# Kernel optimization log

Measured on AMD Instinct MI355X. Metric: run time of the kernel, lower is better.

Reference implementation:

```python
import jax, jax.numpy as jnp
import numpy as np

B, S, M, D, H, L, FF = 2, 1024, 1024, 512, 8, 4, 2048
HD = D // H  # head dim 64
EPS = 1e-6   # fast_transformers linear-attention eps
LN_EPS = 1e-5


def setup_inputs() -> dict:
    key = jax.random.key(0)
    keys = iter(jax.random.split(key, 64))
    def w(shape, s=0.02):
        return jax.random.normal(next(keys), shape, dtype=jnp.float32) * s
    inp = {
        "memory": jax.random.normal(next(keys), (B, M, D), dtype=jnp.float32),
        "target": jax.random.normal(next(keys), (B, S, D), dtype=jnp.float32),
    }
    for p in ("sa", "ca"):
        for n in ("q", "k", "v", "o"):
            inp[f"{p}_W{n}"] = w((L, D, D))
            inp[f"{p}_b{n}"] = jnp.zeros((L, D), jnp.float32)
    inp["ff_W1"] = w((L, D, FF)); inp["ff_b1"] = jnp.zeros((L, FF), jnp.float32)
    inp["ff_W2"] = w((L, FF, D)); inp["ff_b2"] = jnp.zeros((L, D), jnp.float32)
    for n in ("ln1", "ln2", "ln3"):
        inp[f"{n}_g"] = jnp.ones((L, D), jnp.float32)
        inp[f"{n}_b"] = jnp.zeros((L, D), jnp.float32)
    inp["lnf_g"] = jnp.ones((D,), jnp.float32)
    inp["lnf_b"] = jnp.zeros((D,), jnp.float32)
    return inp


def _ln(x, g, b):
    m = x.mean(-1, keepdims=True)
    v = ((x - m) ** 2).mean(-1, keepdims=True)
    return (x - m) / jnp.sqrt(v + LN_EPS) * g + b


def _phi(x):  # elu feature map: elu(x) + 1
    return jax.nn.elu(x) + 1.0


def _heads(x, W, b):  # [b,s,D] -> [b,s,H,HD]
    y = x @ W + b
    return y.reshape(y.shape[0], y.shape[1], H, HD)


def _causal_linear_attn(q, k, v):
    # q,k already feature-mapped. cumulative KV state per step.
    kv = jnp.cumsum(jnp.einsum('bshd,bshm->bshdm', k, v), axis=1)  # [B,S,H,HD,HD]
    z = jnp.cumsum(k, axis=1)                                      # [B,S,H,HD]
    num = jnp.einsum('bshd,bshdm->bshm', q, kv)
    den = jnp.einsum('bshd,bshd->bsh', q, z) + EPS
    return num / den[..., None]


def _cross_linear_attn(q, k, v):
    kv = jnp.einsum('bmhd,bmhv->bhdv', k, v)  # [B,H,HD,HD]
    z = k.sum(axis=1)                          # [B,H,HD]
    num = jnp.einsum('bshd,bhdv->bshv', q, kv)
    den = jnp.einsum('bshd,bhd->bsh', q, z) + EPS
    return num / den[..., None]


def reference(memory, target,
              sa_Wq, sa_bq, sa_Wk, sa_bk, sa_Wv, sa_bv, sa_Wo, sa_bo,
              ca_Wq, ca_bq, ca_Wk, ca_bk, ca_Wv, ca_bv, ca_Wo, ca_bo,
              ff_W1, ff_b1, ff_W2, ff_b2,
              ln1_g, ln1_b, ln2_g, ln2_b, ln3_g, ln3_b, lnf_g, lnf_b):
    x = target
    for i in range(L):
        # causal linear self-attention
        q = _phi(_heads(x, sa_Wq[i], sa_bq[i]))
        k = _phi(_heads(x, sa_Wk[i], sa_bk[i]))
        v = _heads(x, sa_Wv[i], sa_bv[i])
        a = _causal_linear_attn(q, k, v).reshape(B, S, D) @ sa_Wo[i] + sa_bo[i]
        x = _ln(x + a, ln1_g[i], ln1_b[i])
        # linear cross-attention over memory
        q = _phi(_heads(x, ca_Wq[i], ca_bq[i]))
        k = _phi(_heads(memory, ca_Wk[i], ca_bk[i]))
        v = _heads(memory, ca_Wv[i], ca_bv[i])
        a = _cross_linear_attn(q, k, v).reshape(B, S, D) @ ca_Wo[i] + ca_bo[i]
        x = _ln(x + a, ln2_g[i], ln2_b[i])
        # gelu FFN
        y = jax.nn.gelu(x @ ff_W1[i] + ff_b1[i], approximate=False) @ ff_W2[i] + ff_b2[i]
        x = _ln(x + y, ln3_g[i], ln3_b[i])
    return _ln(x, lnf_g, lnf_b)
```

## Files before the change

### kernel.cpp

```cpp
#include <hip/hip_runtime.h>
#include <hip/hip_bf16.h>
#include <math.h>


typedef unsigned short u16;
typedef __bf16 bf16x8 __attribute__((ext_vector_type(8)));
typedef float f32x4v __attribute__((ext_vector_type(4)));
typedef long long i64;

#define DEVI __device__ __forceinline__

DEVI float bf2f(u16 u) { return __uint_as_float(((unsigned)u) << 16); }
DEVI u16 f2bf(float f) {
  unsigned u = __float_as_uint(f);
  u += 0x7FFFu + ((u >> 16) & 1u);
  return (u16)(u >> 16);
}

struct P8i { const float* p[8]; };
struct P8o { u16* p[8]; };

__global__ __launch_bounds__(256) void transpose_b8(P8i in, P8o out)
{
  __shared__ float tile[64 * 65];
  const int m = blockIdx.z;
  const int set = m >> 2, layer = m & 3;
  const float* src = in.p[set] + (size_t)layer * 512 * 512;
  u16* dst = out.p[set] + (size_t)layer * 512 * 512;
  const int n0 = blockIdx.x * 64, k0 = blockIdx.y * 64;
  const int t = threadIdx.x;
#pragma unroll
  for (int p = 0; p < 16; ++p) {
    const int e = t + p * 256;
    const int lk = e >> 6, ln = e & 63;
    tile[lk * 65 + ln] = src[(size_t)(k0 + lk) * 512 + n0 + ln];
  }
  __syncthreads();
#pragma unroll
  for (int p = 0; p < 16; ++p) {
    const int e = t + p * 256;
    const int ln = e >> 6, lk = e & 63;
    dst[(size_t)(n0 + ln) * 512 + k0 + lk] = f2bf(tile[lk * 65 + ln]);
  }
}

__global__ __launch_bounds__(256) void transpose_f2b(
    const float* __restrict__ in, u16* __restrict__ out, int K, int N)
{
  __shared__ float tile[64 * 65];
  const size_t mat = (size_t)blockIdx.z * K * N;
  const int n0 = blockIdx.x * 64, k0 = blockIdx.y * 64;
  const int t = threadIdx.x;
#pragma unroll
  for (int p = 0; p < 16; ++p) {
    const int e = t + p * 256;
    const int lk = e >> 6, ln = e & 63;
    tile[lk * 65 + ln] = in[mat + (size_t)(k0 + lk) * N + n0 + ln];
  }
  __syncthreads();
#pragma unroll
  for (int p = 0; p < 16; ++p) {
    const int e = t + p * 256;
    const int ln = e >> 6, lk = e & 63;
    out[mat + (size_t)(n0 + ln) * K + k0 + lk] = f2bf(tile[lk * 65 + ln]);
  }
}

__global__ __launch_bounds__(256) void cast_dual(
    const float* __restrict__ in, float* __restrict__ fout, u16* __restrict__ bout)
{
  const int i = blockIdx.x * 256 + threadIdx.x;
  const float4 a = ((const float4*)in)[i * 2];
  const float4 b = ((const float4*)in)[i * 2 + 1];
  if (fout) {
    ((float4*)fout)[i * 2] = a;
    ((float4*)fout)[i * 2 + 1] = b;
  }
  ((ushort4*)bout)[i * 2]     = make_ushort4(f2bf(a.x), f2bf(a.y), f2bf(a.z), f2bf(a.w));
  ((ushort4*)bout)[i * 2 + 1] = make_ushort4(f2bf(b.x), f2bf(b.y), f2bf(b.z), f2bf(b.w));
}

template<int CDT>
__global__ __launch_bounds__(256, 4) void gemm64(
    const u16* __restrict__ A0, const u16* __restrict__ A1, const u16* __restrict__ A2,
    const u16* __restrict__ W0, const u16* __restrict__ W1, const u16* __restrict__ W2,
    const float* __restrict__ b0, const float* __restrict__ b1, const float* __restrict__ b2,
    void* __restrict__ C0, void* __restrict__ C1, void* __restrict__ C2,
    int acts, int N, int K, int lda, int ldw, int lognyb,
    i64 zA, i64 zW, i64 zB, i64 zC, int biasAllZ)
{
  constexpr int LDT = 72;
  __shared__ __align__(16) u16 As[2][64 * LDT];
  __shared__ __align__(16) u16 Bs[2][64 * LDT];
  const int tid = threadIdx.x;
  const int by = blockIdx.y;
  const int z = blockIdx.z;
  const int seg = by >> lognyb;
  const int ny = by & ((1 << lognyb) - 1);
  const u16* A = (seg == 0 ? A0 : (seg == 1 ? A1 : A2)) + (size_t)z * zA;
  const u16* W = (seg == 0 ? W0 : (seg == 1 ? W1 : W2)) + (size_t)z * zW;
  const float* bias = (seg == 0 ? b0 : (seg == 1 ? b1 : b2)) + (size_t)z * zB;
  void* Cv = seg == 0 ? C0 : (seg == 1 ? C1 : C2);
  const int act = (acts >> (2 * seg)) & 3;
  const bool dobias = biasAllZ || (z == 0);

  const int bm0 = blockIdx.x * 64, bn0 = ny * 64;
  const int lane = tid & 63, wid = tid >> 6;
  const int wr = wid >> 1, wc = wid & 1;
  const int l15 = lane & 15, lg = lane >> 4;
  const int srow = tid >> 2, scg = (tid & 3) * 16;
  const u16* Ap = A + (size_t)(bm0 + srow) * lda + scg;
  const u16* Wp = W + (size_t)(bn0 + srow) * ldw + scg;
  const int nk = K >> 6;

  uint4 a00, a01, b00, b01;
  uint4 a10, a11, b10, b11;
#define LDSET0(k) { a00 = *(const uint4*)(Ap + (k) * 64); a01 = *(const uint4*)(Ap + (k) * 64 + 8); \
                    b00 = *(const uint4*)(Wp + (k) * 64); b01 = *(const uint4*)(Wp + (k) * 64 + 8); }
#define LDSET1(k) { a10 = *(const uint4*)(Ap + (k) * 64); a11 = *(const uint4*)(Ap + (k) * 64 + 8); \
                    b10 = *(const uint4*)(Wp + (k) * 64); b11 = *(const uint4*)(Wp + (k) * 64 + 8); }
#define STSET0(buf) { *(uint4*)&As[buf][srow * LDT + scg] = a00; *(uint4*)&As[buf][srow * LDT + scg + 8] = a01; \
                      *(uint4*)&Bs[buf][srow * LDT + scg] = b00; *(uint4*)&Bs[buf][srow * LDT + scg + 8] = b01; }
#define STSET1(buf) { *(uint4*)&As[buf][srow * LDT + scg] = a10; *(uint4*)&As[buf][srow * LDT + scg + 8] = a11; \
                      *(uint4*)&Bs[buf][srow * LDT + scg] = b10; *(uint4*)&Bs[buf][srow * LDT + scg + 8] = b11; }

  f32x4v acc[2][2] = {};
  auto mfma_on = [&](int buf) {
    bf16x8 af[2][2], bw[2][2];
#pragma unroll
    for (int kk = 0; kk < 2; ++kk) {
#pragma unroll
      for (int mm = 0; mm < 2; ++mm)
        af[kk][mm] = *(const bf16x8*)&As[buf][(wr * 32 + mm * 16 + l15) * LDT + kk * 32 + lg * 8];
#pragma unroll
      for (int nn = 0; nn < 2; ++nn)
        bw[kk][nn] = *(const bf16x8*)&Bs[buf][(wc * 32 + nn * 16 + l15) * LDT + kk * 32 + lg * 8];
    }
#pragma unroll
    for (int kk = 0; kk < 2; ++kk)
#pragma unroll
      for (int mm = 0; mm < 2; ++mm)
#pragma unroll
        for (int nn = 0; nn < 2; ++nn)
          acc[mm][nn] = __builtin_amdgcn_mfma_f32_16x16x32_bf16(af[kk][mm], bw[kk][nn], acc[mm][nn], 0, 0, 0);
  };

  LDSET0(0); STSET0(0);
  LDSET1(1);
  __syncthreads();
  for (int k = 0; k < nk; k += 2) {
    if (k + 2 < nk) LDSET0(k + 2);
    mfma_on(0);
    STSET1(1);
    __syncthreads();
    if (k + 3 < nk) LDSET1(k + 3);
    mfma_on(1);
    if (k + 2 < nk) STSET0(0);
    __syncthreads();
  }
#undef LDSET0
#undef LDSET1
#undef STSET0
#undef STSET1
#pragma unroll
  for (int nn = 0; nn < 2; ++nn) {
    const int col = bn0 + wc * 32 + nn * 16 + l15;
    const float bv = dobias ? bias[col] : 0.f;
#pragma unroll
    for (int mm = 0; mm < 2; ++mm) {
#pragma unroll
      for (int r = 0; r < 4; ++r) {
        const int row = bm0 + wr * 32 + mm * 16 + lg * 4 + r;
        float v = acc[mm][nn][r] + bv;
        if (act == 1) v = v > 0.f ? v + 1.f : __expf(v);
        else if (act == 2) v = 0.5f * v * (1.f + erff(v * 0.70710678f));
        const size_t idx = (size_t)row * N + col + (size_t)z * zC;
        if (CDT == 0) ((float*)Cv)[idx] = v;
        else          ((u16*)Cv)[idx] = f2bf(v);
      }
    }
  }
}

__global__ __launch_bounds__(256) void lin_chunk_mfma(
    const u16* __restrict__ kbuf, const u16* __restrict__ vbuf,
    float* __restrict__ KVc, float* __restrict__ zc)
{
  constexpr int LDT = 72;
  __shared__ __align__(16) u16 Kt[64 * LDT];
  __shared__ __align__(16) u16 Vt[64 * LDT];
  const int c = blockIdx.x, bh = blockIdx.y, zl = blockIdx.z;
  kbuf += (size_t)zl * 2048 * 512;
  vbuf += (size_t)zl * 2048 * 512;
  KVc  += (size_t)zl * 16 * 16 * 4096;
  zc   += (size_t)zl * 16 * 16 * 64;
  const int b = bh >> 3, h = bh & 7;
  const int t = threadIdx.x;
  const size_t rowbase = (size_t)(b * 1024 + c * 64);
  const int sp = t >> 4, colq = (t & 15) * 4;
#pragma unroll
  for (int pp = 0; pp < 2; ++pp) {
    const int s0 = pp * 32 + 2 * sp;
    const ushort4 ka = *(const ushort4*)&kbuf[(rowbase + s0) * 512 + h * 64 + colq];
    const ushort4 kb_ = *(const ushort4*)&kbuf[(rowbase + s0 + 1) * 512 + h * 64 + colq];
    const ushort4 va = *(const ushort4*)&vbuf[(rowbase + s0) * 512 + h * 64 + colq];
    const ushort4 vb_ = *(const ushort4*)&vbuf[(rowbase + s0 + 1) * 512 + h * 64 + colq];
    *(unsigned*)&Kt[(colq + 0) * LDT + s0] = (unsigned)ka.x | ((unsigned)kb_.x << 16);
    *(unsigned*)&Kt[(colq + 1) * LDT + s0] = (unsigned)ka.y | ((unsigned)kb_.y << 16);
    *(unsigned*)&Kt[(colq + 2) * LDT + s0] = (unsigned)ka.z | ((unsigned)kb_.z << 16);
    *(unsigned*)&Kt[(colq + 3) * LDT + s0] = (unsigned)ka.w | ((unsigned)kb_.w << 16);
    *(unsigned*)&Vt[(colq + 0) * LDT + s0] = (unsigned)va.x | ((unsigned)vb_.x << 16);
    *(unsigned*)&Vt[(colq + 1) * LDT + s0] = (unsigned)va.y | ((unsigned)vb_.y << 16);
    *(unsigned*)&Vt[(colq + 2) * LDT + s0] = (unsigned)va.z | ((unsigned)vb_.z << 16);
    *(unsigned*)&Vt[(colq + 3) * LDT + s0] = (unsigned)va.w | ((unsigned)vb_.w << 16);
  }
  __syncthreads();
  {
    const int zd = t >> 2, zg = t & 3;
    float zp = 0.f;
#pragma unroll
    for (int ss = 0; ss < 16; ++ss) zp += bf2f(Kt[zd * LDT + zg * 16 + ss]);
    zp += __shfl_xor(zp, 1, 64);
    zp += __shfl_xor(zp, 2, 64);
    if (zg == 0) zc[(size_t)(bh * 16 + c) * 64 + zd] = zp;
  }
  const int lane = t & 63, wid = t >> 6;
  const int wr = wid >> 1, wc = wid & 1;
  const int l15 = lane & 15, lg = lane >> 4;
  bf16x8 av[2][2], bk[2][2];
#pragma unroll
  for (int kk = 0; kk < 2; ++kk) {
#pragma unroll
    for (int mm = 0; mm < 2; ++mm)
      av[kk][mm] = *(const bf16x8*)&Vt[(wr * 32 + mm * 16 + l15) * LDT + kk * 32 + lg * 8];
#pragma unroll
    for (int nn = 0; nn < 2; ++nn)
      bk[kk][nn] = *(const bf16x8*)&Kt[(wc * 32 + nn * 16 + l15) * LDT + kk * 32 + lg * 8];
  }
  f32x4v acc[2][2] = {};
#pragma unroll
  for (int kk = 0; kk < 2; ++kk)
#pragma unroll
    for (int mm = 0; mm < 2; ++mm)
#pragma unroll
      for (int nn = 0; nn < 2; ++nn)
        acc[mm][nn] = __builtin_amdgcn_mfma_f32_16x16x32_bf16(av[kk][mm], bk[kk][nn], acc[mm][nn], 0, 0, 0);
  float* kvout = KVc + (size_t)(bh * 16 + c) * 4096;
#pragma unroll
  for (int mm = 0; mm < 2; ++mm)
#pragma unroll
    for (int r = 0; r < 4; ++r) {
      const int row = wr * 32 + mm * 16 + lg * 4 + r;
#pragma unroll
      for (int nn = 0; nn < 2; ++nn) {
        const int col = wc * 32 + nn * 16 + l15;
        kvout[row * 64 + col] = acc[mm][nn][r];
      }
    }
}

__global__ __launch_bounds__(256) void sa_apply_mfma(
    const u16* __restrict__ qbuf, const u16* __restrict__ kbuf,
    const u16* __restrict__ vbuf, const float* __restrict__ KVc,
    const float* __restrict__ zc, u16* __restrict__ out)
{
  constexpr int LDT = 72;
  __shared__ __align__(16) u16 Qs[64 * LDT];
  __shared__ __align__(16) u16 Ks[64 * LDT];
  __shared__ __align__(16) u16 Vt[64 * LDT];
  __shared__ __align__(16) u16 Ps[64 * LDT];
  __shared__ __align__(16) u16 KVs[64 * LDT];
  __shared__ float zp[64];
  __shared__ float den1[2][64];
  __shared__ float den2[64];
  const int c = blockIdx.x, bh = blockIdx.y;
  const int b = bh >> 3, h = bh & 7;
  const int t = threadIdx.x;
  const size_t rowbase = (size_t)(b * 1024 + c * 64);
  {
    const int srow = t >> 2, scg = (t & 3) * 16;
    *(uint4*)&Qs[srow * LDT + scg]     = *(const uint4*)&qbuf[(rowbase + srow) * 512 + h * 64 + scg];
    *(uint4*)&Qs[srow * LDT + scg + 8] = *(const uint4*)&qbuf[(rowbase + srow) * 512 + h * 64 + scg + 8];
    *(uint4*)&Ks[srow * LDT + scg]     = *(const uint4*)&kbuf[(rowbase + srow) * 512 + h * 64 + scg];
    *(uint4*)&Ks[srow * LDT + scg + 8] = *(const uint4*)&kbuf[(rowbase + srow) * 512 + h * 64 + scg + 8];
    const float* kvbase = KVc + (size_t)(bh * 16) * 4096 + srow * 64 + scg;
    float4 s0 = make_float4(0, 0, 0, 0), s1 = s0, s2 = s0, s3 = s0;
    for (int cc = 0; cc < c; ++cc) {
      const float* p = kvbase + (size_t)cc * 4096;
      const float4 a0 = *(const float4*)&p[0];
      const float4 a1 = *(const float4*)&p[4];
      const float4 a2 = *(const float4*)&p[8];
      const float4 a3 = *(const float4*)&p[12];
      s0.x += a0.x; s0.y += a0.y; s0.z += a0.z; s0.w += a0.w;
      s1.x += a1.x; s1.y += a1.y; s1.z += a1.z; s1.w += a1.w;
      s2.x += a2.x; s2.y += a2.y; s2.z += a2.z; s2.w += a2.w;
      s3.x += a3.x; s3.y += a3.y; s3.z += a3.z; s3.w += a3.w;
    }
    *(ushort4*)&KVs[srow * LDT + scg + 0]  = make_ushort4(f2bf(s0.x), f2bf(s0.y), f2bf(s0.z), f2bf(s0.w));
    *(ushort4*)&KVs[srow * LDT + scg + 4]  = make_ushort4(f2bf(s1.x), f2bf(s1.y), f2bf(s1.z), f2bf(s1.w));
    *(ushort4*)&KVs[srow * LDT + scg + 8]  = make_ushort4(f2bf(s2.x), f2bf(s2.y), f2bf(s2.z), f2bf(s2.w));
    *(ushort4*)&KVs[srow * LDT + scg + 12] = make_ushort4(f2bf(s3.x), f2bf(s3.y), f2bf(s3.z), f2bf(s3.w));
  }
  {
    const int sp = t >> 4, colq = (t & 15) * 4;
#pragma unroll
    for (int pp = 0; pp < 2; ++pp) {
      const int s0 = pp * 32 + 2 * sp;
      const ushort4 va = *(const ushort4*)&vbuf[(rowbase + s0) * 512 + h * 64 + colq];
      const ushort4 vb_ = *(const ushort4*)&vbuf[(rowbase + s0 + 1) * 512 + h * 64 + colq];
      *(unsigned*)&Vt[(colq + 0) * LDT + s0] = (unsigned)va.x | ((unsigned)vb_.x << 16);
      *(unsigned*)&Vt[(colq + 1) * LDT + s0] = (unsigned)va.y | ((unsigned)vb_.y << 16);
// ... 52 lines not shown
        dsum += val;
      }
      dsum += __shfl_xor(dsum, 1, 64);
      dsum += __shfl_xor(dsum, 2, 64);
      dsum += __shfl_xor(dsum, 4, 64);
      dsum += __shfl_xor(dsum, 8, 64);
      if (l15 == 0) den1[wc][row] = dsum;
    }
  __syncthreads();
  bf16x8 ap[2][2];
#pragma unroll
  for (int kk = 0; kk < 2; ++kk) {
#pragma unroll
    for (int mm = 0; mm < 2; ++mm)
      ap[kk][mm] = *(const bf16x8*)&Ps[(wr * 32 + mm * 16 + l15) * LDT + kk * 32 + lg * 8];
#pragma unroll
    for (int nn = 0; nn < 2; ++nn)
      bx[kk][nn] = *(const bf16x8*)&Vt[(wc * 32 + nn * 16 + l15) * LDT + kk * 32 + lg * 8];
  }
  f32x4v o_acc[2][2] = {};
#pragma unroll
  for (int kk = 0; kk < 2; ++kk)
#pragma unroll
    for (int mm = 0; mm < 2; ++mm)
#pragma unroll
      for (int nn = 0; nn < 2; ++nn)
        o_acc[mm][nn] = __builtin_amdgcn_mfma_f32_16x16x32_bf16(ap[kk][mm], bx[kk][nn], o_acc[mm][nn], 0, 0, 0);
#pragma unroll
  for (int kk = 0; kk < 2; ++kk)
#pragma unroll
    for (int nn = 0; nn < 2; ++nn)
      bx[kk][nn] = *(const bf16x8*)&KVs[(wc * 32 + nn * 16 + l15) * LDT + kk * 32 + lg * 8];
#pragma unroll
  for (int kk = 0; kk < 2; ++kk)
#pragma unroll
    for (int mm = 0; mm < 2; ++mm)
#pragma unroll
      for (int nn = 0; nn < 2; ++nn)
        o_acc[mm][nn] = __builtin_amdgcn_mfma_f32_16x16x32_bf16(af_q[kk][mm], bx[kk][nn], o_acc[mm][nn], 0, 0, 0);
#pragma unroll
  for (int mm = 0; mm < 2; ++mm)
#pragma unroll
    for (int r = 0; r < 4; ++r) {
      const int row = wr * 32 + mm * 16 + lg * 4 + r;
      const float rden = 1.f / (den1[0][row] + den1[1][row] + den2[row] + 1e-6f);
#pragma unroll
      for (int nn = 0; nn < 2; ++nn) {
        const int col = wc * 32 + nn * 16 + l15;
        out[(rowbase + row) * 512 + h * 64 + col] = f2bf(o_acc[mm][nn][r] * rden);
      }
    }
}

__global__ __launch_bounds__(256) void ca_apply_mfma(
    const float* __restrict__ qp0, i64 qstride, const float* __restrict__ KVc,
    const float* __restrict__ zc, u16* __restrict__ out)
{
  constexpr int LDT = 72;
  __shared__ __align__(16) u16 Qs[64 * LDT];
  __shared__ __align__(16) u16 KVs[64 * LDT];
  __shared__ float zt[64];
  __shared__ float den2[64];
  const int c = blockIdx.x, bh = blockIdx.y;
  const int b = bh >> 3, h = bh & 7;
  const int t = threadIdx.x;
  const size_t rowbase = (size_t)(b * 1024 + c * 64);
  {
    const int srow = t >> 2, scg = (t & 3) * 16;
    const float* qa = qp0 + (rowbase + srow) * 512 + h * 64 + scg;
    const float* qb = qa + qstride;
#pragma unroll
    for (int i = 0; i < 4; ++i) {
      const float4 u = *(const float4*)&qa[i * 4];
      const float4 w = *(const float4*)&qb[i * 4];
      float e0 = u.x + w.x, e1 = u.y + w.y, e2 = u.z + w.z, e3 = u.w + w.w;
      e0 = e0 > 0.f ? e0 + 1.f : __expf(e0);
      e1 = e1 > 0.f ? e1 + 1.f : __expf(e1);
      e2 = e2 > 0.f ? e2 + 1.f : __expf(e2);
      e3 = e3 > 0.f ? e3 + 1.f : __expf(e3);
      *(ushort4*)&Qs[srow * LDT + scg + i * 4] = make_ushort4(f2bf(e0), f2bf(e1), f2bf(e2), f2bf(e3));
    }
    const float* kvbase = KVc + (size_t)(bh * 16) * 4096 + srow * 64 + scg;
    float4 s0 = make_float4(0, 0, 0, 0), s1 = s0, s2 = s0, s3 = s0;
    for (int cc = 0; cc < 16; ++cc) {
      const float* p = kvbase + (size_t)cc * 4096;
      const float4 a0 = *(const float4*)&p[0];
      const float4 a1 = *(const float4*)&p[4];
      const float4 a2 = *(const float4*)&p[8];
      const float4 a3 = *(const float4*)&p[12];
      s0.x += a0.x; s0.y += a0.y; s0.z += a0.z; s0.w += a0.w;
      s1.x += a1.x; s1.y += a1.y; s1.z += a1.z; s1.w += a1.w;
      s2.x += a2.x; s2.y += a2.y; s2.z += a2.z; s2.w += a2.w;
      s3.x += a3.x; s3.y += a3.y; s3.z += a3.z; s3.w += a3.w;
    }
    *(ushort4*)&KVs[srow * LDT + scg + 0]  = make_ushort4(f2bf(s0.x), f2bf(s0.y), f2bf(s0.z), f2bf(s0.w));
    *(ushort4*)&KVs[srow * LDT + scg + 4]  = make_ushort4(f2bf(s1.x), f2bf(s1.y), f2bf(s1.z), f2bf(s1.w));
    *(ushort4*)&KVs[srow * LDT + scg + 8]  = make_ushort4(f2bf(s2.x), f2bf(s2.y), f2bf(s2.z), f2bf(s2.w));
    *(ushort4*)&KVs[srow * LDT + scg + 12] = make_ushort4(f2bf(s3.x), f2bf(s3.y), f2bf(s3.z), f2bf(s3.w));
  }
  if (t < 64) {
    float z = 0.f;
    for (int cc = 0; cc < 16; ++cc) z += zc[(size_t)(bh * 16 + cc) * 64 + t];
    zt[t] = z;
  }
  __syncthreads();
  {
    const int di = t >> 2, dg = t & 3;
    float p2 = 0.f;
#pragma unroll
    for (int dd = 0; dd < 16; ++dd)
      p2 += bf2f(Qs[di * LDT + dg * 16 + dd]) * zt[dg * 16 + dd];
    p2 += __shfl_xor(p2, 1, 64);
    p2 += __shfl_xor(p2, 2, 64);
    if (dg == 0) den2[di] = p2;
  }
  const int lane = t & 63, wid = t >> 6;
  const int wr = wid >> 1, wc = wid & 1;
  const int l15 = lane & 15, lg = lane >> 4;
  bf16x8 aq[2][2], bkv[2][2];
#pragma unroll
  for (int kk = 0; kk < 2; ++kk) {
#pragma unroll
    for (int mm = 0; mm < 2; ++mm)
      aq[kk][mm] = *(const bf16x8*)&Qs[(wr * 32 + mm * 16 + l15) * LDT + kk * 32 + lg * 8];
#pragma unroll
    for (int nn = 0; nn < 2; ++nn)
      bkv[kk][nn] = *(const bf16x8*)&KVs[(wc * 32 + nn * 16 + l15) * LDT + kk * 32 + lg * 8];
  }
  f32x4v o_acc[2][2] = {};
#pragma unroll
  for (int kk = 0; kk < 2; ++kk)
#pragma unroll
    for (int mm = 0; mm < 2; ++mm)
#pragma unroll
      for (int nn = 0; nn < 2; ++nn)
        o_acc[mm][nn] = __builtin_amdgcn_mfma_f32_16x16x32_bf16(aq[kk][mm], bkv[kk][nn], o_acc[mm][nn], 0, 0, 0);
  __syncthreads();
#pragma unroll
  for (int mm = 0; mm < 2; ++mm)
#pragma unroll
    for (int r = 0; r < 4; ++r) {
      const int row = wr * 32 + mm * 16 + lg * 4 + r;
      const float rden = 1.f / (den2[row] + 1e-6f);
#pragma unroll
      for (int nn = 0; nn < 2; ++nn) {
        const int col = wc * 32 + nn * 16 + l15;
        out[(rowbase + row) * 512 + h * 64 + col] = f2bf(o_acc[mm][nn][r] * rden);
      }
    }
}

template<int NPART>
__global__ __launch_bounds__(256) void ln_residual(
    float* __restrict__ x, const float* __restrict__ a, i64 pstride,
    const float* __restrict__ g, const float* __restrict__ bt,
    u16* __restrict__ xb)
{
  const int t = threadIdx.x, lane = t & 63, w = t >> 6;
  const int row = blockIdx.x * 4 + w;
  float* xr = x + (size_t)row * 512;
  float4 x0 = *(const float4*)&xr[lane * 8];
  float4 x1 = *(const float4*)&xr[lane * 8 + 4];
  float v[8] = { x0.x, x0.y, x0.z, x0.w, x1.x, x1.y, x1.z, x1.w };
#pragma unroll
  for (int p = 0; p < NPART; ++p) {
    const float* ar = a + (size_t)p * pstride + (size_t)row * 512;
    float4 a0 = *(const float4*)&ar[lane * 8];
    float4 a1 = *(const float4*)&ar[lane * 8 + 4];
    v[0] += a0.x; v[1] += a0.y; v[2] += a0.z; v[3] += a0.w;
    v[4] += a1.x; v[5] += a1.y; v[6] += a1.z; v[7] += a1.w;
  }
  float s = 0.f, sq = 0.f;
#pragma unroll
  for (int i = 0; i < 8; ++i) { s += v[i]; sq += v[i] * v[i]; }
#pragma unroll
  for (int off = 32; off > 0; off >>= 1) {
    s += __shfl_xor(s, off, 64);
    sq += __shfl_xor(sq, off, 64);
  }
  const float mean = s * (1.f / 512.f);
  const float var = sq * (1.f / 512.f) - mean * mean;
  const float rstd = rsqrtf(var + 1e-5f);
  float o[8];
#pragma unroll
  for (int i = 0; i < 8; ++i) {
    const int col = lane * 8 + i;
    o[i] = (v[i] - mean) * rstd * g[col] + bt[col];
  }
  *(float4*)&xr[lane * 8]     = make_float4(o[0], o[1], o[2], o[3]);
  *(float4*)&xr[lane * 8 + 4] = make_float4(o[4], o[5], o[6], o[7]);
  *(ushort4*)&xb[(size_t)row * 512 + lane * 8]     = make_ushort4(f2bf(o[0]), f2bf(o[1]), f2bf(o[2]), f2bf(o[3]));
  *(ushort4*)&xb[(size_t)row * 512 + lane * 8 + 4] = make_ushort4(f2bf(o[4]), f2bf(o[5]), f2bf(o[6]), f2bf(o[7]));
}

__global__ __launch_bounds__(256) void ln_final(
    const float* __restrict__ x, const float* __restrict__ g,
    const float* __restrict__ bt, float* __restrict__ out)
{
  const int t = threadIdx.x, lane = t & 63, w = t >> 6;
  const int row = blockIdx.x * 4 + w;
  const float* xr = x + (size_t)row * 512;
  float4 x0 = *(const float4*)&xr[lane * 8];
  float4 x1 = *(const float4*)&xr[lane * 8 + 4];
  float v[8] = { x0.x, x0.y, x0.z, x0.w, x1.x, x1.y, x1.z, x1.w };
// ... 11 lines not shown
  float o[8];
#pragma unroll
  for (int i = 0; i < 8; ++i) {
    const int col = lane * 8 + i;
    o[i] = (v[i] - mean) * rstd * g[col] + bt[col];
  }
  *(float4*)&out[(size_t)row * 512 + lane * 8]     = make_float4(o[0], o[1], o[2], o[3]);
  *(float4*)&out[(size_t)row * 512 + lane * 8 + 4] = make_float4(o[4], o[5], o[6], o[7]);
}

extern "C" void kernel_launch(void* const* d_in, const int* in_sizes, int n_in,
                              void* d_out, int out_size, void* d_ws, size_t ws_size,
                              hipStream_t stream)
{
  (void)in_sizes; (void)n_in; (void)out_size; (void)ws_size;
  constexpr int Dm = 512, Lc = 4, FFc = 2048;
  constexpr i64 TOK = 2048LL * 512;

  const float* memory = (const float*)d_in[0];
  const float* target = (const float*)d_in[1];
  const float *saW[4], *sab[4], *caW[4], *cab[4];
  for (int j = 0; j < 4; ++j) {
    saW[j] = (const float*)d_in[2 + 2 * j];
    sab[j] = (const float*)d_in[3 + 2 * j];
    caW[j] = (const float*)d_in[10 + 2 * j];
    cab[j] = (const float*)d_in[11 + 2 * j];
  }
  const float* ffW1 = (const float*)d_in[18];
  const float* ffb1 = (const float*)d_in[19];
  const float* ffW2 = (const float*)d_in[20];
  const float* ffb2 = (const float*)d_in[21];
  const float* lng[4] = { (const float*)d_in[22], (const float*)d_in[24],
                          (const float*)d_in[26], (const float*)d_in[28] };
  const float* lnb[4] = { (const float*)d_in[23], (const float*)d_in[25],
                          (const float*)d_in[27], (const float*)d_in[29] };

  size_t off = 0;
  auto alloc = [&](size_t bytes) -> void* {
    void* p = (char*)d_ws + off;
    off += (bytes + 255) & ~(size_t)255;
    return p;
  };
  u16* WtS[4]; u16* WtC[4];
  for (int j = 0; j < 4; ++j) WtS[j] = (u16*)alloc((size_t)Lc * Dm * Dm * 2);
  for (int j = 0; j < 4; ++j) WtC[j] = (u16*)alloc((size_t)Lc * Dm * Dm * 2);
  u16* WtF1 = (u16*)alloc((size_t)Lc * Dm * FFc * 2);
  u16* WtF2 = (u16*)alloc((size_t)Lc * FFc * Dm * 2);
  float* x     = (float*)alloc(TOK * 4);
  u16*   xb    = (u16*)alloc(TOK * 2);
  u16*   memb  = (u16*)alloc(TOK * 2);
  u16*   qh    = (u16*)alloc(TOK * 2);
  u16*   kh    = (u16*)alloc(TOK * 2);
  u16*   vh    = (u16*)alloc(TOK * 2);
  u16*   khAll = (u16*)alloc((size_t)Lc * TOK * 2);
  u16*   vhAll = (u16*)alloc((size_t)Lc * TOK * 2);
  float* resid = (float*)alloc((size_t)4 * TOK * 4);
  u16*   attn  = (u16*)alloc(TOK * 2);
  u16*   ffh   = (u16*)alloc((size_t)2048 * 2048 * 2);
  float* KVc   = (float*)alloc((size_t)16 * 16 * 4096 * 4);
  float* zcb   = (float*)alloc((size_t)16 * 16 * 64 * 4);
  float* KVcA  = (float*)alloc((size_t)Lc * 16 * 16 * 4096 * 4);
  float* zcbA  = (float*)alloc((size_t)Lc * 16 * 16 * 64 * 4);

  {
    P8i pin; P8o pout;
    for (int j = 0; j < 4; ++j) { pin.p[j] = saW[j]; pout.p[j] = WtS[j]; }
    for (int j = 0; j < 4; ++j) { pin.p[4 + j] = caW[j]; pout.p[4 + j] = WtC[j]; }
    transpose_b8<<<dim3(8, 8, 32), 256, 0, stream>>>(pin, pout);
  }
  transpose_f2b<<<dim3(32, 8, 4), 256, 0, stream>>>(ffW1, WtF1, Dm, FFc);
  transpose_f2b<<<dim3(8, 32, 4), 256, 0, stream>>>(ffW2, WtF2, FFc, Dm);

  cast_dual<<<512, 256, 0, stream>>>(target, x, xb);
  cast_dual<<<512, 256, 0, stream>>>(memory, nullptr, memb);

  gemm64<1><<<dim3(32, 16, 4), 256, 0, stream>>>(
      memb, memb, memb, WtC[1], WtC[2], WtC[2],
      cab[1], cab[2], cab[2], khAll, vhAll, vhAll,
      0x01, 512, 512, 512, 512, 3,
      0, (i64)Dm * Dm, (i64)Dm, TOK, 1);
  lin_chunk_mfma<<<dim3(16, 16, 4), 256, 0, stream>>>(khAll, vhAll, KVcA, zcbA);

  for (int i = 0; i < Lc; ++i) {
    const size_t wo  = (size_t)i * Dm * Dm;
    const size_t wo1 = (size_t)i * Dm * FFc;
    const size_t wo2 = (size_t)i * FFc * Dm;
    gemm64<1><<<dim3(32, 24), 256, 0, stream>>>(
        xb, xb, xb, WtS[0] + wo, WtS[1] + wo, WtS[2] + wo,
        sab[0] + i * Dm, sab[1] + i * Dm, sab[2] + i * Dm,
        qh, kh, vh, 0x05, 512, 512, 512, 512, 3, 0, 0, 0, 0, 1);
    lin_chunk_mfma<<<dim3(16, 16), 256, 0, stream>>>(kh, vh, KVc, zcb);
    sa_apply_mfma<<<dim3(16, 16), 256, 0, stream>>>(qh, kh, vh, KVc, zcb, attn);
    gemm64<0><<<dim3(32, 8, 2), 256, 0, stream>>>(
        attn, attn, attn, WtS[3] + wo, WtS[3] + wo, WtS[3] + wo,
        sab[3] + i * Dm, sab[3] + i * Dm, sab[3] + i * Dm,
        resid, resid, resid, 0, 512, 256, 512, 512, 3,
        256, 256, 0, TOK, 0);
    ln_residual<2><<<512, 256, 0, stream>>>(x, resid, TOK, lng[0] + i * Dm, lnb[0] + i * Dm, xb);
    gemm64<0><<<dim3(32, 8, 2), 256, 0, stream>>>(
        xb, xb, xb, WtC[0] + wo, WtC[0] + wo, WtC[0] + wo,
        cab[0] + i * Dm, cab[0] + i * Dm, cab[0] + i * Dm,
        resid, resid, resid, 0, 512, 256, 512, 512, 3,
        256, 256, 0, TOK, 0);
    ca_apply_mfma<<<dim3(16, 16), 256, 0, stream>>>(
        resid, TOK, KVcA + (size_t)i * 16 * 16 * 4096, zcbA + (size_t)i * 16 * 16 * 64, attn);
    gemm64<0><<<dim3(32, 8, 2), 256, 0, stream>>>(
        attn, attn, attn, WtC[3] + wo, WtC[3] + wo, WtC[3] + wo,
        cab[3] + i * Dm, cab[3] + i * Dm, cab[3] + i * Dm,
        resid, resid, resid, 0, 512, 256, 512, 512, 3,
        256, 256, 0, TOK, 0);
    ln_residual<2><<<512, 256, 0, stream>>>(x, resid, TOK, lng[1] + i * Dm, lnb[1] + i * Dm, xb);
    gemm64<1><<<dim3(32, 32), 256, 0, stream>>>(
        xb, xb, xb, WtF1 + wo1, WtF1 + wo1, WtF1 + wo1,
        ffb1 + i * FFc, ffb1 + i * FFc, ffb1 + i * FFc,
        ffh, ffh, ffh, 2, 2048, 512, 512, 512, 5, 0, 0, 0, 0, 1);
    gemm64<0><<<dim3(32, 8, 4), 256, 0, stream>>>(
        ffh, ffh, ffh, WtF2 + wo2, WtF2 + wo2, WtF2 + wo2,
        ffb2 + i * Dm, ffb2 + i * Dm, ffb2 + i * Dm,
        resid, resid, resid, 0, 512, 512, 2048, 2048, 3,
        512, 512, 0, TOK, 0);
    ln_residual<4><<<512, 256, 0, stream>>>(x, resid, TOK, lng[2] + i * Dm, lnb[2] + i * Dm, xb);
  }
  ln_final<<<512, 256, 0, stream>>>(x, lng[3], lnb[3], (float*)d_out);
}
```

Measured before the change: 593.7 us.

## Fuse head projections with chunk KV-state computation and cross-attn Q apply

Adds a proj_chunk kernel that computes Q/K/V head projections per 64-row tile and one head, then immediately builds the chunk K^T V state and the z sums from shared memory. This replaces the separate projection GEMM plus lin_chunk_mfma, for both memory K/V and self-attention. A caq_apply kernel fuses the cross-attention Q projection, without split-K, with the KV application, and the two cast kernels merge into one launch. The aim is fewer launches and less intermediate global traffic. The cost is lower per-block parallelism: blocks now run serial projections with occupancy hint 2, and the memory K/V head outputs are no longer written.

```diff
diff --git a/kernel.cpp b/kernel.cpp
--- a/kernel.cpp
+++ b/kernel.cpp
@@ -66,18 +66,282 @@
   }
 }
 
-__global__ __launch_bounds__(256) void cast_dual(
-    const float* __restrict__ in, float* __restrict__ fout, u16* __restrict__ bout)
-{
-  const int i = blockIdx.x * 256 + threadIdx.x;
-  const float4 a = ((const float4*)in)[i * 2];
-  const float4 b = ((const float4*)in)[i * 2 + 1];
-  if (fout) {
-    ((float4*)fout)[i * 2] = a;
-    ((float4*)fout)[i * 2 + 1] = b;
-  }
-  ((ushort4*)bout)[i * 2]     = make_ushort4(f2bf(a.x), f2bf(a.y), f2bf(a.z), f2bf(a.w));
-  ((ushort4*)bout)[i * 2 + 1] = make_ushort4(f2bf(b.x), f2bf(b.y), f2bf(b.z), f2bf(b.w));
+__global__ __launch_bounds__(256) void cast_both(
+    const float* __restrict__ target, const float* __restrict__ memory,
+    float* __restrict__ x, u16* __restrict__ xb, u16* __restrict__ memb)
+{
+  if (blockIdx.x < 512) {
+    const int i = blockIdx.x * 256 + threadIdx.x;
+    const float4 a = ((const float4*)target)[i * 2];
+    const float4 b = ((const float4*)target)[i * 2 + 1];
+    ((float4*)x)[i * 2] = a;
+    ((float4*)x)[i * 2 + 1] = b;
+    ((ushort4*)xb)[i * 2]     = make_ushort4(f2bf(a.x), f2bf(a.y), f2bf(a.z), f2bf(a.w));
+    ((ushort4*)xb)[i * 2 + 1] = make_ushort4(f2bf(b.x), f2bf(b.y), f2bf(b.z), f2bf(b.w));
+  } else {
+    const int i = (blockIdx.x - 512) * 256 + threadIdx.x;
+    const float4 a = ((const float4*)memory)[i * 2];
+    const float4 b = ((const float4*)memory)[i * 2 + 1];
+    ((ushort4*)memb)[i * 2]     = make_ushort4(f2bf(a.x), f2bf(a.y), f2bf(a.z), f2bf(a.w));
+    ((ushort4*)memb)[i * 2 + 1] = make_ushort4(f2bf(b.x), f2bf(b.y), f2bf(b.z), f2bf(b.w));
+  }
+}
+
+#define GEMM512(APTR, WPTR)                                                    \
+  {                                                                            \
+    uint4 ra0 = *(const uint4*)(APTR);                                         \
+    uint4 ra1 = *(const uint4*)((APTR) + 8);                                   \
+    uint4 rb0 = *(const uint4*)(WPTR);                                         \
+    uint4 rb1 = *(const uint4*)((WPTR) + 8);                                   \
+    *(uint4*)&As[0][srow * LDT + scg] = ra0;                                   \
+    *(uint4*)&As[0][srow * LDT + scg + 8] = ra1;                               \
+    *(uint4*)&Bs[0][srow * LDT + scg] = rb0;                                   \
+    *(uint4*)&Bs[0][srow * LDT + scg + 8] = rb1;                               \
+    __syncthreads();                                                           \
+    int cur = 0;                                                               \
+    for (int k0 = 0; k0 < 512; k0 += 64) {                                     \
+      const bool more = (k0 + 64 < 512);                                       \
+      if (more) {                                                              \
+        ra0 = *(const uint4*)((APTR) + k0 + 64);                               \
+        ra1 = *(const uint4*)((APTR) + k0 + 72);                               \
+        rb0 = *(const uint4*)((WPTR) + k0 + 64);                               \
+        rb1 = *(const uint4*)((WPTR) + k0 + 72);                               \
+      }                                                                        \
+      bf16x8 af[2][2], bw[2][2];                                               \
+      _Pragma("unroll")                                                        \
+      for (int kk = 0; kk < 2; ++kk) {                                         \
+        _Pragma("unroll")                                                      \
+        for (int mm = 0; mm < 2; ++mm)                                         \
+          af[kk][mm] = *(const bf16x8*)&As[cur][(wr * 32 + mm * 16 + l15) * LDT + kk * 32 + lg * 8]; \
+        _Pragma("unroll")                                                      \
+        for (int nn = 0; nn < 2; ++nn)                                         \
+          bw[kk][nn] = *(const bf16x8*)&Bs[cur][(wc * 32 + nn * 16 + l15) * LDT + kk * 32 + lg * 8]; \
+      }                                                                        \
+      _Pragma("unroll")                                                        \
+      for (int kk = 0; kk < 2; ++kk)                                           \
+        _Pragma("unroll")                                                      \
+        for (int mm = 0; mm < 2; ++mm)                                         \
+          _Pragma("unroll")                                                    \
+          for (int nn = 0; nn < 2; ++nn)                                       \
+            acc[mm][nn] = __builtin_amdgcn_mfma_f32_16x16x32_bf16(af[kk][mm], bw[kk][nn], acc[mm][nn], 0, 0, 0); \
+      if (more) {                                                              \
+        *(uint4*)&As[cur ^ 1][srow * LDT + scg] = ra0;                         \
+        *(uint4*)&As[cur ^ 1][srow * LDT + scg + 8] = ra1;                     \
+        *(uint4*)&Bs[cur ^ 1][srow * LDT + scg] = rb0;                         \
+        *(uint4*)&Bs[cur ^ 1][srow * LDT + scg + 8] = rb1;                     \
+      }                                                                        \
+      __syncthreads();                                                         \
+      cur ^= 1;                                                                \
+    }                                                                          \
+  }
+
+template<int NPROJ>
+__global__ __launch_bounds__(256, 2) void proj_chunk(
+    const u16* __restrict__ xbuf,
+    const u16* __restrict__ W0p, const u16* __restrict__ W1p, const u16* __restrict__ W2p,
+    const float* __restrict__ b0p, const float* __restrict__ b1p, const float* __restrict__ b2p,
+    u16* __restrict__ o0, u16* __restrict__ o1, u16* __restrict__ o2,
+    float* __restrict__ KVc, float* __restrict__ zc,
+    i64 zW, i64 zB, i64 zKV, i64 zZ)
+{
+  constexpr int LDT = 72;
+  __shared__ __align__(16) u16 As[2][64 * LDT];
+  __shared__ __align__(16) u16 Bs[2][64 * LDT];
+  __shared__ __align__(16) u16 Kt[64 * LDT];
+  __shared__ __align__(16) u16 Vt[64 * LDT];
+  const int tid = threadIdx.x;
+  const int rowblk = blockIdx.x, head = blockIdx.y, z = blockIdx.z;
+  const int c = rowblk & 15, bh = (rowblk >> 4) * 8 + head;
+  const int lane = tid & 63, wid = tid >> 6;
+  const int wr = wid >> 1, wc = wid & 1;
+  const int l15 = lane & 15, lg = lane >> 4;
+  const int srow = tid >> 2, scg = (tid & 3) * 16;
+  const size_t rowbase = (size_t)rowblk * 64;
+  const u16* Ap = xbuf + (rowbase + srow) * 512 + scg;
+
+  const u16* Ws[3] = { W0p, W1p, W2p };
+  const float* bs[3] = { b0p, b1p, b2p };
+  u16* os[3] = { o0, o1, o2 };
+
+#pragma unroll
+  for (int p = 0; p < NPROJ; ++p) {
+    const u16* Wp = Ws[p] + (size_t)z * zW + (size_t)(head * 64 + srow) * 512 + scg;
+    const float* bp = bs[p] + (size_t)z * zB + head * 64;
+    u16* op = os[p];
+    const bool actphi = (p != NPROJ - 1);
+    const bool toK = (p == NPROJ - 2), toV = (p == NPROJ - 1);
+    f32x4v acc[2][2] = {};
+    GEMM512(Ap, Wp);
+#pragma unroll
+    for (int nn = 0; nn < 2; ++nn) {
+      const int col = wc * 32 + nn * 16 + l15;
+      const float bv = bp[col];
+#pragma unroll
+      for (int mm = 0; mm < 2; ++mm) {
+#pragma unroll
+        for (int r = 0; r < 4; ++r) {
+          const int row = wr * 32 + mm * 16 + lg * 4 + r;
+          float v = acc[mm][nn][r] + bv;
+          if (actphi) v = v > 0.f ? v + 1.f : __expf(v);
+          const u16 hv = f2bf(v);
+          if (op) op[(rowbase + row) * 512 + head * 64 + col] = hv;
+          if (toK) Kt[col * LDT + row] = hv;
+          if (toV) Vt[col * LDT + row] = hv;
+        }
+      }
+    }
+  }
+  __syncthreads();
+  float* KVcp = KVc + (size_t)z * zKV + (size_t)(bh * 16 + c) * 4096;
+  float* zcp  = zc  + (size_t)z * zZ  + (size_t)(bh * 16 + c) * 64;
+  {
+    const int zd = tid >> 2, zg = tid & 3;
+    float zp = 0.f;
+#pragma unroll
+    for (int ss = 0; ss < 16; ++ss) zp += bf2f(Kt[zd * LDT + zg * 16 + ss]);
+    zp += __shfl_xor(zp, 1, 64);
+    zp += __shfl_xor(zp, 2, 64);
+    if (zg == 0) zcp[zd] = zp;
+  }
+  bf16x8 av[2][2], bk[2][2];
+#pragma unroll
+  for (int kk = 0; kk < 2; ++kk) {
+#pragma unroll
+    for (int mm = 0; mm < 2; ++mm)
+      av[kk][mm] = *(const bf16x8*)&Vt[(wr * 32 + mm * 16 + l15) * LDT + kk * 32 + lg * 8];
+#pragma unroll
+    for (int nn = 0; nn < 2; ++nn)
+      bk[kk][nn] = *(const bf16x8*)&Kt[(wc * 32 + nn * 16 + l15) * LDT + kk * 32 + lg * 8];
+  }
+  f32x4v kacc[2][2] = {};
+#pragma unroll
+  for (int kk = 0; kk < 2; ++kk)
+#pragma unroll
+    for (int mm = 0; mm < 2; ++mm)
+#pragma unroll
+      for (int nn = 0; nn < 2; ++nn)
+        kacc[mm][nn] = __builtin_amdgcn_mfma_f32_16x16x32_bf16(av[kk][mm], bk[kk][nn], kacc[mm][nn], 0, 0, 0);
+#pragma unroll
+  for (int mm = 0; mm < 2; ++mm)
+#pragma unroll
+    for (int r = 0; r < 4; ++r) {
+      const int row = wr * 32 + mm * 16 + lg * 4 + r;
+#pragma unroll
+      for (int nn = 0; nn < 2; ++nn) {
+        const int col = wc * 32 + nn * 16 + l15;
+        KVcp[row * 64 + col] = kacc[mm][nn][r];
+      }
+    }
+}
+
+__global__ __launch_bounds__(256, 2) void caq_apply(
+    const u16* __restrict__ xbuf, const u16* __restrict__ Wq,
+    const float* __restrict__ bq, const float* __restrict__ KVc,
+    const float* __restrict__ zc, u16* __restrict__ out)
+{
+  constexpr int LDT = 72;
+  __shared__ __align__(16) u16 As[2][64 * LDT];
+  __shared__ __align__(16) u16 Bs[2][64 * LDT];
+  __shared__ __align__(16) u16 Qs[64 * LDT];
+  __shared__ __align__(16) u16 KVs[64 * LDT];
+  __shared__ float zt[64];
+  __shared__ float den2[64];
+  const int tid = threadIdx.x;
+  const int rowblk = blockIdx.x, head = blockIdx.y;
+  const int bh = (rowblk >> 4) * 8 + head;
+  const int lane = tid & 63, wid = tid >> 6;
+  const int wr = wid >> 1, wc = wid & 1;
+  const int l15 = lane & 15, lg = lane >> 4;
+  const int srow = tid >> 2, scg = (tid & 3) * 16;
+  const size_t rowbase = (size_t)rowblk * 64;
+  const u16* Ap = xbuf + (rowbase + srow) * 512 + scg;
+  const u16* Wp = Wq + (size_t)(head * 64 + srow) * 512 + scg;
+
+  {
+    const float* kvbase = KVc + (size_t)(bh * 16) * 4096 + srow * 64 + scg;
+    float4 s0 = make_float4(0, 0, 0, 0), s1 = s0, s2 = s0, s3 = s0;
+    for (int cc = 0; cc < 16; ++cc) {
+      const float* p = kvbase + (size_t)cc * 4096;
+      const float4 a0 = *(const float4*)&p[0];
+      const float4 a1 = *(const float4*)&p[4];
+      const float4 a2 = *(const float4*)&p[8];
+      const float4 a3 = *(const float4*)&p[12];
+      s0.x += a0.x; s0.y += a0.y; s0.z += a0.z; s0.w += a0.w;
+      s1.x += a1.x; s1.y += a1.y; s1.z += a1.z; s1.w += a1.w;
+      s2.x += a2.x; s2.y += a2.y; s2.z += a2.z; s2.w += a2.w;
+      s3.x += a3.x; s3.y += a3.y; s3.z += a3.z; s3.w += a3.w;
+    }
+    *(ushort4*)&KVs[srow * LDT + scg + 0]  = make_ushort4(f2bf(s0.x), f2bf(s0.y), f2bf(s0.z), f2bf(s0.w));
+    *(ushort4*)&KVs[srow * LDT + scg + 4]  = make_ushort4(f2bf(s1.x), f2bf(s1.y), f2bf(s1.z), f2bf(s1.w));
+    *(ushort4*)&KVs[srow * LDT + scg + 8]  = make_ushort4(f2bf(s2.x), f2bf(s2.y), f2bf(s2.z), f2bf(s2.w));
+    *(ushort4*)&KVs[srow * LDT + scg + 12] = make_ushort4(f2bf(s3.x), f2bf(s3.y), f2bf(s3.z), f2bf(s3.w));
+  }
+  if (tid < 64) {
+    float zsum = 0.f;
+    for (int cc = 0; cc < 16; ++cc) zsum += zc[(size_t)(bh * 16 + cc) * 64 + tid];
+    zt[tid] = zsum;
+  }
+
+  f32x4v acc[2][2] = {};
+  GEMM512(Ap, Wp);
+
+#pragma unroll
+  for (int nn = 0; nn < 2; ++nn) {
+    const int col = wc * 32 + nn * 16 + l15;
+    const float bv = bq[head * 64 + col];
+#pragma unroll
+    for (int mm = 0; mm < 2; ++mm) {
+#pragma unroll
+      for (int r = 0; r < 4; ++r) {
+        const int row = wr * 32 + mm * 16 + lg * 4 + r;
+        float v = acc[mm][nn][r] + bv;
+        v = v > 0.f ? v + 1.f : __expf(v);
+        Qs[row * LDT + col] = f2bf(v);
+      }
+    }
+  }
+  __syncthreads();
+  {
+    const int di = tid >> 2, dg = tid & 3;
+    float p2 = 0.f;
+#pragma unroll
+    for (int dd = 0; dd < 16; ++dd)
+      p2 += bf2f(Qs[di * LDT + dg * 16 + dd]) * zt[dg * 16 + dd];
+    p2 += __shfl_xor(p2, 1, 64);
+    p2 += __shfl_xor(p2, 2, 64);
+    if (dg == 0) den2[di] = p2;
+  }
+  bf16x8 aq[2][2], bkv[2][2];
+#pragma unroll
+  for (int kk = 0; kk < 2; ++kk) {
+#pragma unroll
+    for (int mm = 0; mm < 2; ++mm)
+      aq[kk][mm] = *(const bf16x8*)&Qs[(wr * 32 + mm * 16 + l15) * LDT + kk * 32 + lg * 8];
+#pragma unroll
+    for (int nn = 0; nn < 2; ++nn)
+      bkv[kk][nn] = *(const bf16x8*)&KVs[(wc * 32 + nn * 16 + l15) * LDT + kk * 32 + lg * 8];
+  }
+  f32x4v o_acc[2][2] = {};
+#pragma unroll
+  for (int kk = 0; kk < 2; ++kk)
+#pragma unroll
+    for (int mm = 0; mm < 2; ++mm)
+#pragma unroll
+      for (int nn = 0; nn < 2; ++nn)
+        o_acc[mm][nn] = __builtin_amdgcn_mfma_f32_16x16x32_bf16(aq[kk][mm], bkv[kk][nn], o_acc[mm][nn], 0, 0, 0);
+  __syncthreads();
+#pragma unroll
+  for (int mm = 0; mm < 2; ++mm)
+#pragma unroll
+    for (int r = 0; r < 4; ++r) {
+      const int row = wr * 32 + mm * 16 + lg * 4 + r;
+      const float rden = 1.f / (den2[row] + 1e-6f);
+#pragma unroll
+      for (int nn = 0; nn < 2; ++nn) {
+        const int col = wc * 32 + nn * 16 + l15;
+        out[(rowbase + row) * 512 + head * 64 + col] = f2bf(o_acc[mm][nn][r] * rden);
+      }
+    }
 }
 
 template<int CDT>
@@ -180,83 +444,6 @@
       }
     }
   }
-}
-
-__global__ __launch_bounds__(256) void lin_chunk_mfma(
-    const u16* __restrict__ kbuf, const u16* __restrict__ vbuf,
-    float* __restrict__ KVc, float* __restrict__ zc)
-{
-  constexpr int LDT = 72;
-  __shared__ __align__(16) u16 Kt[64 * LDT];
-  __shared__ __align__(16) u16 Vt[64 * LDT];
-  const int c = blockIdx.x, bh = blockIdx.y, zl = blockIdx.z;
-  kbuf += (size_t)zl * 2048 * 512;
-  vbuf += (size_t)zl * 2048 * 512;
-  KVc  += (size_t)zl * 16 * 16 * 4096;
-  zc   += (size_t)zl * 16 * 16 * 64;
-  const int b = bh >> 3, h = bh & 7;
-  const int t = threadIdx.x;
-  const size_t rowbase = (size_t)(b * 1024 + c * 64);
-  const int sp = t >> 4, colq = (t & 15) * 4;
-#pragma unroll
-  for (int pp = 0; pp < 2; ++pp) {
-    const int s0 = pp * 32 + 2 * sp;
-    const ushort4 ka = *(const ushort4*)&kbuf[(rowbase + s0) * 512 + h * 64 + colq];
-    const ushort4 kb_ = *(const ushort4*)&kbuf[(rowbase + s0 + 1) * 512 + h * 64 + colq];
-    const ushort4 va = *(const ushort4*)&vbuf[(rowbase + s0) * 512 + h * 64 + colq];
-    const ushort4 vb_ = *(const ushort4*)&vbuf[(rowbase + s0 + 1) * 512 + h * 64 + colq];
-    *(unsigned*)&Kt[(colq + 0) * LDT + s0] = (unsigned)ka.x | ((unsigned)kb_.x << 16);
-    *(unsigned*)&Kt[(colq + 1) * LDT + s0] = (unsigned)ka.y | ((unsigned)kb_.y << 16);
-    *(unsigned*)&Kt[(colq + 2) * LDT + s0] = (unsigned)ka.z | ((unsigned)kb_.z << 16);
-    *(unsigned*)&Kt[(colq + 3) * LDT + s0] = (unsigned)ka.w | ((unsigned)kb_.w << 16);
-    *(unsigned*)&Vt[(colq + 0) * LDT + s0] = (unsigned)va.x | ((unsigned)vb_.x << 16);
-    *(unsigned*)&Vt[(colq + 1) * LDT + s0] = (unsigned)va.y | ((unsigned)vb_.y << 16);
-    *(unsigned*)&Vt[(colq + 2) * LDT + s0] = (unsigned)va.z | ((unsigned)vb_.z << 16);
-    *(unsigned*)&Vt[(colq + 3) * LDT + s0] = (unsigned)va.w | ((unsigned)vb_.w << 16);
-  }
-  __syncthreads();
-  {
-    const int zd = t >> 2, zg = t & 3;
-    float zp = 0.f;
-#pragma unroll
-    for (int ss = 0; ss < 16; ++ss) zp += bf2f(Kt[zd * LDT + zg * 16 + ss]);
-    zp += __shfl_xor(zp, 1, 64);
-    zp += __shfl_xor(zp, 2, 64);
-    if (zg == 0) zc[(size_t)(bh * 16 + c) * 64 + zd] = zp;
-  }
-  const int lane = t & 63, wid = t >> 6;
-  const int wr = wid >> 1, wc = wid & 1;
-  const int l15 = lane & 15, lg = lane >> 4;
-  bf16x8 av[2][2], bk[2][2];
-#pragma unroll
-  for (int kk = 0; kk < 2; ++kk) {
-#pragma unroll
-    for (int mm = 0; mm < 2; ++mm)
-      av[kk][mm] = *(const bf16x8*)&Vt[(wr * 32 + mm * 16 + l15) * LDT + kk * 32 + lg * 8];
-#pragma unroll
-    for (int nn = 0; nn < 2; ++nn)
-      bk[kk][nn] = *(const bf16x8*)&Kt[(wc * 32 + nn * 16 + l15) * LDT + kk * 32 + lg * 8];
-  }
-  f32x4v acc[2][2] = {};
-#pragma unroll
-  for (int kk = 0; kk < 2; ++kk)
-#pragma unroll
-    for (int mm = 0; mm < 2; ++mm)
-#pragma unroll
-      for (int nn = 0; nn < 2; ++nn)
-        acc[mm][nn] = __builtin_amdgcn_mfma_f32_16x16x32_bf16(av[kk][mm], bk[kk][nn], acc[mm][nn], 0, 0, 0);
-  float* kvout = KVc + (size_t)(bh * 16 + c) * 4096;
-#pragma unroll
-  for (int mm = 0; mm < 2; ++mm)
-#pragma unroll
-    for (int r = 0; r < 4; ++r) {
-      const int row = wr * 32 + mm * 16 + lg * 4 + r;
-#pragma unroll
-      for (int nn = 0; nn < 2; ++nn) {
-        const int col = wc * 32 + nn * 16 + l15;
-        kvout[row * 64 + col] = acc[mm][nn][r];
-      }
-    }
 }
 
 __global__ __launch_bounds__(256) void sa_apply_mfma(
@@ -415,104 +602,6 @@
     }
 }
 
-__global__ __launch_bounds__(256) void ca_apply_mfma(
-    const float* __restrict__ qp0, i64 qstride, const float* __restrict__ KVc,
-    const float* __restrict__ zc, u16* __restrict__ out)
-{
-  constexpr int LDT = 72;
-  __shared__ __align__(16) u16 Qs[64 * LDT];
-  __shared__ __align__(16) u16 KVs[64 * LDT];
-  __shared__ float zt[64];
-  __shared__ float den2[64];
-  const int c = blockIdx.x, bh = blockIdx.y;
-  const int b = bh >> 3, h = bh & 7;
-  const int t = threadIdx.x;
-  const size_t rowbase = (size_t)(b * 1024 + c * 64);
-  {
-    const int srow = t >> 2, scg = (t & 3) * 16;
-    const float* qa = qp0 + (rowbase + srow) * 512 + h * 64 + scg;
-    const float* qb = qa + qstride;
-#pragma unroll
-    for (int i = 0; i < 4; ++i) {
-      const float4 u = *(const float4*)&qa[i * 4];
-      const float4 w = *(const float4*)&qb[i * 4];
-      float e0 = u.x + w.x, e1 = u.y + w.y, e2 = u.z + w.z, e3 = u.w + w.w;
-      e0 = e0 > 0.f ? e0 + 1.f : __expf(e0);
-      e1 = e1 > 0.f ? e1 + 1.f : __expf(e1);
-      e2 = e2 > 0.f ? e2 + 1.f : __expf(e2);
-      e3 = e3 > 0.f ? e3 + 1.f : __expf(e3);
-      *(ushort4*)&Qs[srow * LDT + scg + i * 4] = make_ushort4(f2bf(e0), f2bf(e1), f2bf(e2), f2bf(e3));
-    }
-    const float* kvbase = KVc + (size_t)(bh * 16) * 4096 + srow * 64 + scg;
-    float4 s0 = make_float4(0, 0, 0, 0), s1 = s0, s2 = s0, s3 = s0;
-    for (int cc = 0; cc < 16; ++cc) {
-      const float* p = kvbase + (size_t)cc * 4096;
-      const float4 a0 = *(const float4*)&p[0];
-      const float4 a1 = *(const float4*)&p[4];
-      const float4 a2 = *(const float4*)&p[8];
-      const float4 a3 = *(const float4*)&p[12];
-      s0.x += a0.x; s0.y += a0.y; s0.z += a0.z; s0.w += a0.w;
-      s1.x += a1.x; s1.y += a1.y; s1.z += a1.z; s1.w += a1.w;
-      s2.x += a2.x; s2.y += a2.y; s2.z += a2.z; s2.w += a2.w;
-      s3.x += a3.x; s3.y += a3.y; s3.z += a3.z; s3.w += a3.w;
-    }
-    *(ushort4*)&KVs[srow * LDT + scg + 0]  = make_ushort4(f2bf(s0.x), f2bf(s0.y), f2bf(s0.z), f2bf(s0.w));
-    *(ushort4*)&KVs[srow * LDT + scg + 4]  = make_ushort4(f2bf(s1.x), f2bf(s1.y), f2bf(s1.z), f2bf(s1.w));
-    *(ushort4*)&KVs[srow * LDT + scg + 8]  = make_ushort4(f2bf(s2.x), f2bf(s2.y), f2bf(s2.z), f2bf(s2.w));
-    *(ushort4*)&KVs[srow * LDT + scg + 12] = make_ushort4(f2bf(s3.x), f2bf(s3.y), f2bf(s3.z), f2bf(s3.w));
-  }
-  if (t < 64) {
-    float z = 0.f;
-    for (int cc = 0; cc < 16; ++cc) z += zc[(size_t)(bh * 16 + cc) * 64 + t];
-    zt[t] = z;
-  }
-  __syncthreads();
-  {
-    const int di = t >> 2, dg = t & 3;
-    float p2 = 0.f;
-#pragma unroll
-    for (int dd = 0; dd < 16; ++dd)
-      p2 += bf2f(Qs[di * LDT + dg * 16 + dd]) * zt[dg * 16 + dd];
-    p2 += __shfl_xor(p2, 1, 64);
-    p2 += __shfl_xor(p2, 2, 64);
-    if (dg == 0) den2[di] = p2;
-  }
-  const int lane = t & 63, wid = t >> 6;
-  const int wr = wid >> 1, wc = wid & 1;
-  const int l15 = lane & 15, lg = lane >> 4;
-  bf16x8 aq[2][2], bkv[2][2];
-#pragma unroll
-  for (int kk = 0; kk < 2; ++kk) {
-#pragma unroll
-    for (int mm = 0; mm < 2; ++mm)
-      aq[kk][mm] = *(const bf16x8*)&Qs[(wr * 32 + mm * 16 + l15) * LDT + kk * 32 + lg * 8];
-#pragma unroll
-    for (int nn = 0; nn < 2; ++nn)
-      bkv[kk][nn] = *(const bf16x8*)&KVs[(wc * 32 + nn * 16 + l15) * LDT + kk * 32 + lg * 8];
-  }
-  f32x4v o_acc[2][2] = {};
-#pragma unroll
-  for (int kk = 0; kk < 2; ++kk)
-#pragma unroll
-    for (int mm = 0; mm < 2; ++mm)
-#pragma unroll
-      for (int nn = 0; nn < 2; ++nn)
-        o_acc[mm][nn] = __builtin_amdgcn_mfma_f32_16x16x32_bf16(aq[kk][mm], bkv[kk][nn], o_acc[mm][nn], 0, 0, 0);
-  __syncthreads();
-#pragma unroll
-  for (int mm = 0; mm < 2; ++mm)
-#pragma unroll
-    for (int r = 0; r < 4; ++r) {
-      const int row = wr * 32 + mm * 16 + lg * 4 + r;
-      const float rden = 1.f / (den2[row] + 1e-6f);
-#pragma unroll
-      for (int nn = 0; nn < 2; ++nn) {
-        const int col = wc * 32 + nn * 16 + l15;
-        out[(rowbase + row) * 512 + h * 64 + col] = f2bf(o_acc[mm][nn][r] * rden);
-      }
-    }
-}
-
 template<int NPART>
 __global__ __launch_bounds__(256) void ln_residual(
     float* __restrict__ x, const float* __restrict__ a, i64 pstride,
@@ -630,8 +719,6 @@
   u16*   qh    = (u16*)alloc(TOK * 2);
   u16*   kh    = (u16*)alloc(TOK * 2);
   u16*   vh    = (u16*)alloc(TOK * 2);
-  u16*   khAll = (u16*)alloc((size_t)Lc * TOK * 2);
-  u16*   vhAll = (u16*)alloc((size_t)Lc * TOK * 2);
   float* resid = (float*)alloc((size_t)4 * TOK * 4);
   u16*   attn  = (u16*)alloc(TOK * 2);
   u16*   ffh   = (u16*)alloc((size_t)2048 * 2048 * 2);
@@ -649,25 +736,21 @@
   transpose_f2b<<<dim3(32, 8, 4), 256, 0, stream>>>(ffW1, WtF1, Dm, FFc);
   transpose_f2b<<<dim3(8, 32, 4), 256, 0, stream>>>(ffW2, WtF2, FFc, Dm);
 
-  cast_dual<<<512, 256, 0, stream>>>(target, x, xb);
-  cast_dual<<<512, 256, 0, stream>>>(memory, nullptr, memb);
-
-  gemm64<1><<<dim3(32, 16, 4), 256, 0, stream>>>(
-      memb, memb, memb, WtC[1], WtC[2], WtC[2],
-      cab[1], cab[2], cab[2], khAll, vhAll, vhAll,
-      0x01, 512, 512, 512, 512, 3,
-      0, (i64)Dm * Dm, (i64)Dm, TOK, 1);
-  lin_chunk_mfma<<<dim3(16, 16, 4), 256, 0, stream>>>(khAll, vhAll, KVcA, zcbA);
+  cast_both<<<1024, 256, 0, stream>>>(target, memory, x, xb, memb);
+
+  proj_chunk<2><<<dim3(32, 8, 4), 256, 0, stream>>>(
+      memb, WtC[1], WtC[2], WtC[2], cab[1], cab[2], cab[2],
+      nullptr, nullptr, nullptr, KVcA, zcbA,
+      (i64)Dm * Dm, (i64)Dm, (i64)16 * 16 * 4096, (i64)16 * 16 * 64);
 
   for (int i = 0; i < Lc; ++i) {
     const size_t wo  = (size_t)i * Dm * Dm;
     const size_t wo1 = (size_t)i * Dm * FFc;
     const size_t wo2 = (size_t)i * FFc * Dm;
-    gemm64<1><<<dim3(32, 24), 256, 0, stream>>>(
-        xb, xb, xb, WtS[0] + wo, WtS[1] + wo, WtS[2] + wo,
+    proj_chunk<3><<<dim3(32, 8, 1), 256, 0, stream>>>(
+        xb, WtS[0] + wo, WtS[1] + wo, WtS[2] + wo,
         sab[0] + i * Dm, sab[1] + i * Dm, sab[2] + i * Dm,
-        qh, kh, vh, 0x05, 512, 512, 512, 512, 3, 0, 0, 0, 0, 1);
-    lin_chunk_mfma<<<dim3(16, 16), 256, 0, stream>>>(kh, vh, KVc, zcb);
+        qh, kh, vh, KVc, zcb, 0, 0, 0, 0);
     sa_apply_mfma<<<dim3(16, 16), 256, 0, stream>>>(qh, kh, vh, KVc, zcb, attn);
     gemm64<0><<<dim3(32, 8, 2), 256, 0, stream>>>(
         attn, attn, attn, WtS[3] + wo, WtS[3] + wo, WtS[3] + wo,
@@ -675,13 +758,9 @@
         resid, resid, resid, 0, 512, 256, 512, 512, 3,
         256, 256, 0, TOK, 0);
     ln_residual<2><<<512, 256, 0, stream>>>(x, resid, TOK, lng[0] + i * Dm, lnb[0] + i * Dm, xb);
-    gemm64<0><<<dim3(32, 8, 2), 256, 0, stream>>>(
-        xb, xb, xb, WtC[0] + wo, WtC[0] + wo, WtC[0] + wo,
-        cab[0] + i * Dm, cab[0] + i * Dm, cab[0] + i * Dm,
-        resid, resid, resid, 0, 512, 256, 512, 512, 3,
-        256, 256, 0, TOK, 0);
-    ca_apply_mfma<<<dim3(16, 16), 256, 0, stream>>>(
-        resid, TOK, KVcA + (size_t)i * 16 * 16 * 4096, zcbA + (size_t)i * 16 * 16 * 64, attn);
+    caq_apply<<<dim3(32, 8), 256, 0, stream>>>(
+        xb, WtC[0] + wo, cab[0] + i * Dm,
+        KVcA + (size_t)i * 16 * 16 * 4096, zcbA + (size_t)i * 16 * 16 * 64, attn);
     gemm64<0><<<dim3(32, 8, 2), 256, 0, stream>>>(
         attn, attn, attn, WtC[3] + wo, WtC[3] + wo, WtC[3] + wo,
         cab[3] + i * Dm, cab[3] + i * Dm, cab[3] + i * Dm,
```

Result: no change. 602.8 us (+1.5%).
